# Performance work log

Hardware: AMD Instinct MI355X
Metric: run time of the kernel (lower is better)

The kernel has to match this reference:

```python
import jax, jax.numpy as jnp
import numpy as np

N_EMBD = 1024
N_HEAD = 16

def setup_inputs() -> dict:
    key = jax.random.key(0)
    ks = jax.random.split(key, 5)
    C = N_EMBD
    x = jax.random.normal(ks[0], (4, 2048, C), dtype=jnp.float32)
    s = 1.0 / np.sqrt(C)
    W_attn = jax.random.normal(ks[1], (C, 3 * C), dtype=jnp.float32) * s
    b_attn = jnp.zeros((3 * C,), dtype=jnp.float32)
    W_proj = jax.random.normal(ks[2], (C, C), dtype=jnp.float32) * s
    b_proj = jnp.zeros((C,), dtype=jnp.float32)
    return {"x": x, "W_attn": W_attn, "b_attn": b_attn, "W_proj": W_proj, "b_proj": b_proj}

def reference(x, W_attn, b_attn, W_proj, b_proj):
    B, S, C = x.shape
    Nh = N_HEAD
    Ne = C // Nh
    qkv = x @ W_attn + b_attn                      # [B,S,3C]
    q, k, v = jnp.split(qkv, 3, axis=-1)
    def heads(t):
        return t.reshape(B, S, Nh, Ne).transpose(0, 2, 1, 3)  # [B,Nh,S,Ne]
    q, k, v = heads(q), heads(k), heads(v)
    scale = 1.0 / np.sqrt(Ne)
    att = scale * jnp.einsum('bhqe,bhke->bhqk', q, k)          # [B,Nh,S,S]
    mask = jnp.tril(jnp.ones((S, S), dtype=bool))
    att = jnp.where(mask, att, -jnp.inf)
    att = jax.nn.softmax(att, axis=-1)
    y = jnp.einsum('bhqk,bhke->bhqe', att, v)                  # [B,Nh,S,Ne]
    y = y.transpose(0, 2, 1, 3).reshape(B, S, C)
    return y @ W_proj + b_proj
```

## Files before the change

### kernel.cpp

```cpp
#include <hip/hip_runtime.h>
#include <cstdint>
#include <cstddef>

typedef _Float16 h16;
typedef _Float16 h16x4 __attribute__((ext_vector_type(4)));
typedef _Float16 h16x8 __attribute__((ext_vector_type(8)));
typedef __fp16 fp16x2 __attribute__((ext_vector_type(2)));
typedef float f32x4 __attribute__((ext_vector_type(4)));

#define LOG2E 1.44269504088896f
#define QSCALE (0.125f * LOG2E)
#define THR 11.0f

static __device__ __forceinline__ f32x4 mfma_f16(h16x8 a, h16x8 b, f32x4 c) {
  return __builtin_amdgcn_mfma_f32_16x16x32_f16(a, b, c, 0, 0, 0);
}

static __device__ __forceinline__ void gload_lds16(const void* g, void* s) {
  __builtin_amdgcn_global_load_lds(
      (__attribute__((address_space(1))) void*)(uintptr_t)g,
      (__attribute__((address_space(3))) void*)s, 16, 0, 0);
}

__global__ __launch_bounds__(256) void k_cvt(const float* __restrict__ in,
                                             h16* __restrict__ out, int n) {
  int i = (blockIdx.x * 256 + threadIdx.x) * 8;
  if (i >= n) return;
  float4 a = *(const float4*)(in + i);
  float4 b = *(const float4*)(in + i + 4);
  h16x8 o;
  o[0] = (h16)a.x; o[1] = (h16)a.y; o[2] = (h16)a.z; o[3] = (h16)a.w;
  o[4] = (h16)b.x; o[5] = (h16)b.y; o[6] = (h16)b.z; o[7] = (h16)b.w;
  *(h16x8*)(out + i) = o;
}

__global__ __launch_bounds__(256) void k_tr_cvt(const float* __restrict__ in,
                                                h16* __restrict__ out, int R, int C) {
  __shared__ float tile[32][33];
  int c0 = blockIdx.x * 32, r0 = blockIdx.y * 32;
  int tx = threadIdx.x & 31, ty = threadIdx.x >> 5;
#pragma unroll
  for (int i = 0; i < 4; i++) {
    int r = ty + i * 8;
    tile[r][tx] = in[(size_t)(r0 + r) * C + c0 + tx];
  }
  __syncthreads();
#pragma unroll
  for (int i = 0; i < 4; i++) {
    int c = ty + i * 8;
    out[(size_t)(c0 + c) * R + r0 + tx] = (h16)tile[tx][c];
  }
}

#define SLOT_H16 24576
#define NT_K 16

static __device__ __forceinline__ void gemm_main256(
    const h16* __restrict__ A, const h16* __restrict__ BT,
    int m0, int n0, h16* sAB, f32x4 acc[4][4]) {
  const int tid = threadIdx.x;
  const int lane = tid & 63, w = tid >> 6;
  const int lm = lane & 15, lh = lane >> 4;
  const int wr = w >> 1, wc = w & 1;
  const int wbase = w * 512;
  const int srow = tid >> 3;
  const int scol = (((tid & 7) ^ (srow & 7)) << 3);
  const h16* gA = A + (size_t)(m0 + srow) * 1024 + scol;
  const h16* gB = BT + (size_t)(n0 + srow) * 1024 + scol;

  auto stage = [&](int t, int sl) {
    const int k = t * 64;
    h16* d = sAB + sl * SLOT_H16 + wbase;
    gload_lds16(gA + (size_t)0 * 65536 + k, d + 0 * 4096);
    gload_lds16(gA + (size_t)1 * 65536 + k, d + 1 * 4096);
    gload_lds16(gA + (size_t)2 * 65536 + k, d + 2 * 4096);
    gload_lds16(gA + (size_t)3 * 65536 + k, d + 3 * 4096);
    gload_lds16(gB + (size_t)0 * 65536 + k, d + 16384 + 0 * 4096);
    gload_lds16(gB + (size_t)1 * 65536 + k, d + 16384 + 1 * 4096);
  };

  stage(0, 0);
  stage(1, 1);
  asm volatile("s_waitcnt vmcnt(6)" ::: "memory");
  __builtin_amdgcn_s_barrier();

  int sl = 0, ss = 2;
  for (int t = 0; t < NT_K; ++t) {
    if (t < NT_K - 2) stage(t + 2, ss);
    const h16* sa = sAB + sl * SLOT_H16;
    const h16* sb = sa + 16384;
    h16x8 af[4][2], bf[4][2];
#pragma unroll
    for (int mi = 0; mi < 4; mi++) {
      const int row = wr * 64 + mi * 16 + lm;
#pragma unroll
      for (int kk = 0; kk < 2; kk++)
        af[mi][kk] = *(const h16x8*)(sa + row * 64 + ((kk * 32 + lh * 8) ^ ((lm & 7) << 3)));
    }
#pragma unroll
    for (int ni = 0; ni < 4; ni++) {
      const int row = wc * 64 + ni * 16 + lm;
#pragma unroll
      for (int kk = 0; kk < 2; kk++)
        bf[ni][kk] = *(const h16x8*)(sb + row * 64 + ((kk * 32 + lh * 8) ^ ((lm & 7) << 3)));
    }
    __builtin_amdgcn_s_setprio(1);
#pragma unroll
    for (int mi = 0; mi < 4; mi++)
#pragma unroll
      for (int ni = 0; ni < 4; ni++)
        acc[mi][ni] = mfma_f16(af[mi][1], bf[ni][1],
                               mfma_f16(af[mi][0], bf[ni][0], acc[mi][ni]));
    __builtin_amdgcn_s_setprio(0);
    if (t < NT_K - 2) asm volatile("s_waitcnt vmcnt(6)" ::: "memory");
    else              asm volatile("s_waitcnt vmcnt(0)" ::: "memory");
    __builtin_amdgcn_s_barrier();
    sl = (sl == 2) ? 0 : sl + 1;
    ss = (ss == 2) ? 0 : ss + 1;
  }
}

__global__ __launch_bounds__(512, 2) void k_gemm_qkv(const h16* __restrict__ xb,
                                                     const h16* __restrict__ WTa,
                                                     const float* __restrict__ b_attn,
                                                     h16* __restrict__ qb,
                                                     h16* __restrict__ kbuf,
                                                     h16* __restrict__ vT) {
  __shared__ __align__(16) h16 sAB[3 * SLOT_H16];
  const int bid = blockIdx.x;
  const int flat = (bid & 7) * 96 + (bid >> 3);
  const int mt = flat / 24, nt = flat % 24;
  const int m0 = mt * 256, n0 = nt * 128;
  f32x4 acc[4][4];
#pragma unroll
  for (int i = 0; i < 4; i++)
#pragma unroll
    for (int j = 0; j < 4; j++) acc[i][j] = (f32x4){0.f, 0.f, 0.f, 0.f};
  gemm_main256(xb, WTa, m0, n0, sAB, acc);

  const int tid = threadIdx.x, lane = tid & 63, w = tid >> 6;
  const int lm = lane & 15, lh = lane >> 4;
  const int wr = w >> 1, wc = w & 1;
#pragma unroll
  for (int ni = 0; ni < 4; ni++) {
    const int n = n0 + wc * 64 + ni * 16 + lm;
    const float bias = b_attn[n];
    const int which = n >> 10, cc = n & 1023, hh = cc >> 6, e = cc & 63;
#pragma unroll
    for (int mi = 0; mi < 4; mi++) {
#pragma unroll
      for (int r = 0; r < 4; r++) {
        const int m = m0 + wr * 64 + mi * 16 + lh * 4 + r;
        const int b = m >> 11, s = m & 2047;
        const h16 o = (h16)(acc[mi][ni][r] + bias);
        const size_t bh = (size_t)(b * 16 + hh);
        if (which == 0)      qb[(bh * 2048 + s) * 64 + e] = o;
        else if (which == 1) kbuf[(bh * 2048 + s) * 64 + e] = o;
        else                 vT[(bh * 64 + e) * 2048 + s] = o;
      }
    }
  }
}

__global__ __launch_bounds__(512, 2) void k_gemm_proj(const h16* __restrict__ yb,
                                                      const h16* __restrict__ WTp,
                                                      const float* __restrict__ b_proj,
                                                      float* __restrict__ out) {
  __shared__ __align__(16) h16 sAB[3 * SLOT_H16];
  const int bid = blockIdx.x;
  const int flat = (bid & 7) * 32 + (bid >> 3);
  const int mt = flat / 8, nt = flat % 8;
  const int m0 = mt * 256, n0 = nt * 128;
  f32x4 acc[4][4];
#pragma unroll
  for (int i = 0; i < 4; i++)
#pragma unroll
    for (int j = 0; j < 4; j++) acc[i][j] = (f32x4){0.f, 0.f, 0.f, 0.f};
  gemm_main256(yb, WTp, m0, n0, sAB, acc);

  const int tid = threadIdx.x, lane = tid & 63, w = tid >> 6;
  const int lm = lane & 15, lh = lane >> 4;
  const int wr = w >> 1, wc = w & 1;
#pragma unroll
  for (int ni = 0; ni < 4; ni++) {
    const int n = n0 + wc * 64 + ni * 16 + lm;
    const float bias = b_proj[n];
#pragma unroll
    for (int mi = 0; mi < 4; mi++) {
#pragma unroll
      for (int r = 0; r < 4; r++) {
        const int m = m0 + wr * 64 + mi * 16 + lh * 4 + r;
        out[(size_t)m * 1024 + n] = acc[mi][ni][r] + bias;
      }
    }
  }
}

__global__ __launch_bounds__(256, 3) void k_attn(const h16* __restrict__ qb,
                                                 const h16* __restrict__ kbuf,
                                                 const h16* __restrict__ vT,
                                                 h16* __restrict__ yb) {
  __shared__ __align__(16) h16 sKt[2][64 * 64];
  __shared__ __align__(16) h16 sVt[2][64 * 64];
  __shared__ __align__(16) h16 sP[4][2][16 * 64];

  const int bid = blockIdx.x;
  const int bh = bid & 63;
  const int qt = 15 - (bid >> 6);
  const int b = bh >> 4, h = bh & 15;
  const int tid = threadIdx.x, lam = tid & 63, w = tid >> 6;
  const int lm = lam & 15, lh = lam >> 4;
  const int q0 = qt * 128 + w * 32;
  const h16* Q = qb + (size_t)bh * 2048 * 64;
  const h16* Kp = kbuf + (size_t)bh * 2048 * 64;
  const h16* Vp = vT + (size_t)bh * 64 * 2048;

  const int srow = lam >> 3;
  const int xo8 = (((lam & 7) ^ (srow & 7)) << 3);

  h16x8 qf[2][2];
#pragma unroll
  for (int rt = 0; rt < 2; rt++)
#pragma unroll
    for (int dc = 0; dc < 2; dc++) {
      h16x8 qv = *(const h16x8*)(Q + (size_t)(q0 + rt * 16 + lm) * 64 + dc * 32 + lh * 8);
      h16x8 o;
#pragma unroll
      for (int i = 0; i < 8; i++) o[i] = (h16)((float)qv[i] * QSCALE);
      qf[rt][dc] = o;
    }

  f32x4 yacc[2][4];
  float m2[2], lw[2];
#pragma unroll
  for (int rt = 0; rt < 2; rt++) {
    m2[rt] = -1e30f;
    lw[rt] = 0.f;
#pragma unroll
    for (int i = 0; i < 4; i++) yacc[rt][i] = (f32x4){0.f, 0.f, 0.f, 0.f};
  }

  const int nsteps = qt * 2 + 2;

#pragma unroll
  for (int i = 0; i < 2; i++) {
    const int seg = 2 * w + i;
    const int r = seg * 8 + srow;
    gload_lds16(Kp + (size_t)r * 64 + xo8, &sKt[0][seg * 512]);
    gload_lds16(Vp + (size_t)r * 2048 + xo8, &sVt[0][seg * 512]);
  }
  asm volatile("s_waitcnt vmcnt(0)" ::: "memory");
  __syncthreads();

  for (int tt = 0; tt < nsteps; ++tt) {
    const int kb0 = tt * 64, cur = tt & 1;
    if (tt + 1 < nsteps) {
      const int kn = kb0 + 64;
#pragma unroll
      for (int i = 0; i < 2; i++) {
        const int seg = 2 * w + i;
        const int r = seg * 8 + srow;
        gload_lds16(Kp + (size_t)(kn + r) * 64 + xo8, &sKt[cur ^ 1][seg * 512]);
        gload_lds16(Vp + (size_t)r * 2048 + kn + xo8, &sVt[cur ^ 1][seg * 512]);
      }
    }
    if (kb0 <= q0 + 31) {
      const bool domask = (kb0 + 63 > q0);
      h16x8 kf[4][2];
#pragma unroll
      for (int ct = 0; ct < 4; ct++)
#pragma unroll
        for (int dc = 0; dc < 2; dc++)
          kf[ct][dc] = *(const h16x8*)(
              &sKt[cur][(ct * 16 + lm) * 64 + ((dc * 32 + lh * 8) ^ ((lm & 7) << 3))]);
      h16x8 vf[4][2];
#pragma unroll
      for (int dt = 0; dt < 4; dt++)
#pragma unroll
        for (int kc = 0; kc < 2; kc++)
          vf[dt][kc] = *(const h16x8*)(
              &sVt[cur][(dt * 16 + lm) * 64 + ((kc * 32 + lh * 8) ^ ((lm & 7) << 3))]);

#pragma unroll
      for (int rt = 0; rt < 2; rt++) {
        const int qrow = q0 + rt * 16 + lm;
        f32x4 sv[4];
        __builtin_amdgcn_s_setprio(1);
#pragma unroll
        for (int ct = 0; ct < 4; ct++) {
          f32x4 s = mfma_f16(kf[ct][0], qf[rt][0], (f32x4){0.f, 0.f, 0.f, 0.f});
          sv[ct] = mfma_f16(kf[ct][1], qf[rt][1], s);
        }
        __builtin_amdgcn_s_setprio(0);
        if (domask) {
#pragma unroll
          for (int ct = 0; ct < 4; ct++)
#pragma unroll
            for (int r = 0; r < 4; r++)
              if (kb0 + ct * 16 + lh * 4 + r > qrow) sv[ct][r] = -1e30f;
        }
        float rm = fmaxf(fmaxf(fmaxf(sv[0][0], sv[0][1]), fmaxf(sv[0][2], sv[0][3])),
                         fmaxf(fmaxf(sv[1][0], sv[1][1]), fmaxf(sv[1][2], sv[1][3])));
        rm = fmaxf(rm, fmaxf(fmaxf(fmaxf(sv[2][0], sv[2][1]), fmaxf(sv[2][2], sv[2][3])),
                             fmaxf(fmaxf(sv[3][0], sv[3][1]), fmaxf(sv[3][2], sv[3][3]))));
        rm = fmaxf(rm, __shfl_xor(rm, 16));
        rm = fmaxf(rm, __shfl_xor(rm, 32));
        if (!__all(rm <= m2[rt] + THR)) {
          const float nm = fmaxf(m2[rt], rm);
          const float alpha = __builtin_amdgcn_exp2f(m2[rt] - nm);
          m2[rt] = nm;
          lw[rt] *= alpha;
#pragma unroll
          for (int dt = 0; dt < 4; dt++) yacc[rt][dt] *= alpha;
        }
        const float m = m2[rt];
        float psum = 0.f;
#pragma unroll
        for (int ct = 0; ct < 4; ct++) {
          const float p0 = __builtin_amdgcn_exp2f(sv[ct][0] - m);
          const float p1 = __builtin_amdgcn_exp2f(sv[ct][1] - m);
          const float p2 = __builtin_amdgcn_exp2f(sv[ct][2] - m);
          const float p3 = __builtin_amdgcn_exp2f(sv[ct][3] - m);
          psum += (p0 + p1) + (p2 + p3);
          const fp16x2 u0 = __builtin_amdgcn_cvt_pkrtz(p0, p1);
          const fp16x2 u1 = __builtin_amdgcn_cvt_pkrtz(p2, p3);
          const int base = ct * 16 + lh * 4;
          *(fp16x2*)(&sP[w][rt][lm * 64 + ((base + 0) ^ ((lm & 7) << 3))]) = u0;
          *(fp16x2*)(&sP[w][rt][lm * 64 + ((base + 2) ^ ((lm & 7) << 3))]) = u1;
        }
        lw[rt] += psum;
      }
#pragma unroll
      for (int rt = 0; rt < 2; rt++) {
        const h16x8 pf0 = *(const h16x8*)(
            &sP[w][rt][lm * 64 + ((lh * 8) ^ ((lm & 7) << 3))]);
        const h16x8 pf1 = *(const h16x8*)(
            &sP[w][rt][lm * 64 + ((32 + lh * 8) ^ ((lm & 7) << 3))]);
        __builtin_amdgcn_s_setprio(1);
#pragma unroll
        for (int dt = 0; dt < 4; dt++) {
          f32x4 y = mfma_f16(vf[dt][0], pf0, yacc[rt][dt]);
          yacc[rt][dt] = mfma_f16(vf[dt][1], pf1, y);
        }
        __builtin_amdgcn_s_setprio(0);
      }
    }
    asm volatile("s_waitcnt vmcnt(0)" ::: "memory");
    __syncthreads();
  }

#pragma unroll
  for (int rt = 0; rt < 2; rt++) {
    float s = lw[rt];
    s += __shfl_xor(s, 16);
    s += __shfl_xor(s, 32);
    const float inv = 1.0f / s;
    const int q = q0 + rt * 16 + lm;
    const size_t yrow = ((size_t)b * 2048 + q) * 1024 + h * 64;
#pragma unroll
    for (int dt = 0; dt < 4; dt++) {
      h16x4 o;
#pragma unroll
      for (int r = 0; r < 4; r++) o[r] = (h16)(yacc[rt][dt][r] * inv);
      *(h16x4*)(yb + yrow + dt * 16 + lh * 4) = o;
    }
  }
}

extern "C" void kernel_launch(void* const* d_in, const int* in_sizes, int n_in,
                              void* d_out, int out_size, void* d_ws, size_t ws_size,
                              hipStream_t stream) {
  const float* x      = (const float*)d_in[0];
  const float* W_attn = (const float*)d_in[1];
  const float* b_attn = (const float*)d_in[2];
  const float* W_proj = (const float*)d_in[3];
  const float* b_proj = (const float*)d_in[4];
  float* out = (float*)d_out;

  char* ws = (char*)d_ws;
  h16* xb   = (h16*)(ws);
  h16* WTa  = (h16*)(ws + 16777216);
  h16* WTp  = (h16*)(ws + 23068672);
  h16* qb   = (h16*)(ws + 25165824);
  h16* kbuf = (h16*)(ws + 41943040);
  h16* vT   = (h16*)(ws + 58720256);
  h16* yb   = xb;

  k_cvt<<<dim3(8192 * 1024 / 2048), 256, 0, stream>>>(x, xb, 8192 * 1024);
  k_tr_cvt<<<dim3(3072 / 32, 1024 / 32), 256, 0, stream>>>(W_attn, WTa, 1024, 3072);
  k_tr_cvt<<<dim3(1024 / 32, 1024 / 32), 256, 0, stream>>>(W_proj, WTp, 1024, 1024);
  k_gemm_qkv<<<dim3(768), 512, 0, stream>>>(xb, WTa, b_attn, qb, kbuf, vT);
  k_attn<<<dim3(64 * 16), 256, 0, stream>>>(qb, kbuf, vT, yb);
  k_gemm_proj<<<dim3(256), 512, 0, stream>>>(yb, WTp, b_proj, out);
}
```

Baseline: 290.9 us.

## Enlarge GEMM tiles to 256x256 with 4-stage K=32 pipeline and split compute phases

Both GEMMs now use 256x256 output tiles per 512-thread block (8 waves as 2x4, 128x64 per wave) instead of 256x128, halving the grid sizes. The K loop uses 32-wide slices with a four-slot LDS ring and three stages in flight, and splits each iteration into two MFMA phases separated by barriers to interleave LDS reads with compute. This aims for more reuse per loaded byte and better latency hiding, at the cost of occupancy of one block per CU and fewer blocks (128 for proj) than CUs on the device.

```diff
diff --git a/kernel.cpp b/kernel.cpp
--- a/kernel.cpp
+++ b/kernel.cpp
@@ -52,105 +52,123 @@
   }
 }
 
-#define SLOT_H16 24576
-#define NT_K 16
-
-static __device__ __forceinline__ void gemm_main256(
-    const h16* __restrict__ A, const h16* __restrict__ BT,
-    int m0, int n0, h16* sAB, f32x4 acc[4][4]) {
+#define SLOT_E 16384
+#define NTK 32
+
+static __device__ __forceinline__ void gemm8p(const h16* __restrict__ A,
+                                              const h16* __restrict__ BT,
+                                              int m0, int n0, h16* sAB,
+                                              f32x4 acc[8][4]) {
   const int tid = threadIdx.x;
   const int lane = tid & 63, w = tid >> 6;
   const int lm = lane & 15, lh = lane >> 4;
-  const int wr = w >> 1, wc = w & 1;
-  const int wbase = w * 512;
-  const int srow = tid >> 3;
-  const int scol = (((tid & 7) ^ (srow & 7)) << 3);
-  const h16* gA = A + (size_t)(m0 + srow) * 1024 + scol;
-  const h16* gB = BT + (size_t)(n0 + srow) * 1024 + scol;
-
-  auto stage = [&](int t, int sl) {
-    const int k = t * 64;
-    h16* d = sAB + sl * SLOT_H16 + wbase;
-    gload_lds16(gA + (size_t)0 * 65536 + k, d + 0 * 4096);
-    gload_lds16(gA + (size_t)1 * 65536 + k, d + 1 * 4096);
-    gload_lds16(gA + (size_t)2 * 65536 + k, d + 2 * 4096);
-    gload_lds16(gA + (size_t)3 * 65536 + k, d + 3 * 4096);
-    gload_lds16(gB + (size_t)0 * 65536 + k, d + 16384 + 0 * 4096);
-    gload_lds16(gB + (size_t)1 * 65536 + k, d + 16384 + 1 * 4096);
+  const int wr = w >> 2, wc = w & 3;
+  const int rdx = (lm >> 1) & 3;
+
+  const h16* pA[2];
+  const h16* pB[2];
+  int dst[2];
+#pragma unroll
+  for (int r = 0; r < 2; r++) {
+    const int idx = tid + r * 512;
+    const int srow = idx >> 2;
+    const int gsrc = (idx & 3) ^ ((srow >> 1) & 3);
+    pA[r] = A + (size_t)(m0 + srow) * 1024 + gsrc * 8;
+    pB[r] = BT + (size_t)(n0 + srow) * 1024 + gsrc * 8;
+    dst[r] = w * 512 + r * 4096;
+  }
+
+  auto stage = [&](int kt) {
+    h16* slot = sAB + (kt & 3) * SLOT_E;
+    const int k0 = kt * 32;
+#pragma unroll
+    for (int r = 0; r < 2; r++) {
+      gload_lds16(pA[r] + k0, slot + dst[r]);
+      gload_lds16(pB[r] + k0, slot + 8192 + dst[r]);
+    }
   };
 
-  stage(0, 0);
-  stage(1, 1);
-  asm volatile("s_waitcnt vmcnt(6)" ::: "memory");
+  stage(0); stage(1); stage(2);
+  asm volatile("s_waitcnt vmcnt(8)" ::: "memory");
   __builtin_amdgcn_s_barrier();
 
-  int sl = 0, ss = 2;
-  for (int t = 0; t < NT_K; ++t) {
-    if (t < NT_K - 2) stage(t + 2, ss);
-    const h16* sa = sAB + sl * SLOT_H16;
-    const h16* sb = sa + 16384;
-    h16x8 af[4][2], bf[4][2];
-#pragma unroll
-    for (int mi = 0; mi < 4; mi++) {
-      const int row = wr * 64 + mi * 16 + lm;
-#pragma unroll
-      for (int kk = 0; kk < 2; kk++)
-        af[mi][kk] = *(const h16x8*)(sa + row * 64 + ((kk * 32 + lh * 8) ^ ((lm & 7) << 3)));
-    }
-#pragma unroll
-    for (int ni = 0; ni < 4; ni++) {
-      const int row = wc * 64 + ni * 16 + lm;
-#pragma unroll
-      for (int kk = 0; kk < 2; kk++)
-        bf[ni][kk] = *(const h16x8*)(sb + row * 64 + ((kk * 32 + lh * 8) ^ ((lm & 7) << 3)));
-    }
+  for (int kt = 0; kt < NTK; ++kt) {
+    if (kt + 3 < NTK) stage(kt + 3);
+    const h16* sa = sAB + (kt & 3) * SLOT_E;
+    const h16* sb = sa + 8192;
+
+    h16x8 af[4], bf[4];
+#pragma unroll
+    for (int mi = 0; mi < 4; mi++)
+      af[mi] = *(const h16x8*)(sa + (wr * 128 + mi * 16 + lm) * 32 + ((lh ^ rdx) << 3));
+#pragma unroll
+    for (int ni = 0; ni < 4; ni++)
+      bf[ni] = *(const h16x8*)(sb + (wc * 64 + ni * 16 + lm) * 32 + ((lh ^ rdx) << 3));
+    __builtin_amdgcn_sched_barrier(0);
+    __builtin_amdgcn_s_barrier();
+    asm volatile("s_waitcnt lgkmcnt(0)" ::: "memory");
     __builtin_amdgcn_s_setprio(1);
 #pragma unroll
     for (int mi = 0; mi < 4; mi++)
 #pragma unroll
       for (int ni = 0; ni < 4; ni++)
-        acc[mi][ni] = mfma_f16(af[mi][1], bf[ni][1],
-                               mfma_f16(af[mi][0], bf[ni][0], acc[mi][ni]));
+        acc[mi][ni] = mfma_f16(af[mi], bf[ni], acc[mi][ni]);
     __builtin_amdgcn_s_setprio(0);
-    if (t < NT_K - 2) asm volatile("s_waitcnt vmcnt(6)" ::: "memory");
-    else              asm volatile("s_waitcnt vmcnt(0)" ::: "memory");
     __builtin_amdgcn_s_barrier();
-    sl = (sl == 2) ? 0 : sl + 1;
-    ss = (ss == 2) ? 0 : ss + 1;
-  }
-}
-
-__global__ __launch_bounds__(512, 2) void k_gemm_qkv(const h16* __restrict__ xb,
+
+    h16x8 ag[4];
+#pragma unroll
+    for (int mi = 0; mi < 4; mi++)
+      ag[mi] = *(const h16x8*)(sa + (wr * 128 + (mi + 4) * 16 + lm) * 32 + ((lh ^ rdx) << 3));
+    __builtin_amdgcn_sched_barrier(0);
+    __builtin_amdgcn_s_barrier();
+    asm volatile("s_waitcnt lgkmcnt(0)" ::: "memory");
+    __builtin_amdgcn_s_setprio(1);
+#pragma unroll
+    for (int mi = 0; mi < 4; mi++)
+#pragma unroll
+      for (int ni = 0; ni < 4; ni++)
+        acc[mi + 4][ni] = mfma_f16(ag[mi], bf[ni], acc[mi + 4][ni]);
+    __builtin_amdgcn_s_setprio(0);
+
+    if (kt < NTK - 3)      asm volatile("s_waitcnt vmcnt(8)" ::: "memory");
+    else if (kt == NTK - 3) asm volatile("s_waitcnt vmcnt(4)" ::: "memory");
+    else if (kt == NTK - 2) asm volatile("s_waitcnt vmcnt(0)" ::: "memory");
+    __builtin_amdgcn_s_barrier();
+  }
+}
+
+__global__ __launch_bounds__(512, 1) void k_gemm_qkv(const h16* __restrict__ xb,
                                                      const h16* __restrict__ WTa,
                                                      const float* __restrict__ b_attn,
                                                      h16* __restrict__ qb,
                                                      h16* __restrict__ kbuf,
                                                      h16* __restrict__ vT) {
-  __shared__ __align__(16) h16 sAB[3 * SLOT_H16];
+  __shared__ __align__(16) h16 sAB[4 * SLOT_E];
   const int bid = blockIdx.x;
-  const int flat = (bid & 7) * 96 + (bid >> 3);
-  const int mt = flat / 24, nt = flat % 24;
-  const int m0 = mt * 256, n0 = nt * 128;
-  f32x4 acc[4][4];
-#pragma unroll
-  for (int i = 0; i < 4; i++)
+  const int flat = (bid & 7) * 48 + (bid >> 3);
+  const int mt = flat / 12, nt = flat % 12;
+  const int m0 = mt * 256, n0 = nt * 256;
+  f32x4 acc[8][4];
+#pragma unroll
+  for (int i = 0; i < 8; i++)
 #pragma unroll
     for (int j = 0; j < 4; j++) acc[i][j] = (f32x4){0.f, 0.f, 0.f, 0.f};
-  gemm_main256(xb, WTa, m0, n0, sAB, acc);
+  gemm8p(xb, WTa, m0, n0, sAB, acc);
 
   const int tid = threadIdx.x, lane = tid & 63, w = tid >> 6;
   const int lm = lane & 15, lh = lane >> 4;
-  const int wr = w >> 1, wc = w & 1;
+  const int wr = w >> 2, wc = w & 3;
 #pragma unroll
   for (int ni = 0; ni < 4; ni++) {
     const int n = n0 + wc * 64 + ni * 16 + lm;
     const float bias = b_attn[n];
     const int which = n >> 10, cc = n & 1023, hh = cc >> 6, e = cc & 63;
 #pragma unroll
-    for (int mi = 0; mi < 4; mi++) {
+    for (int mi = 0; mi < 8; mi++) {
 #pragma unroll
       for (int r = 0; r < 4; r++) {
-        const int m = m0 + wr * 64 + mi * 16 + lh * 4 + r;
+        const int m = m0 + wr * 128 + mi * 16 + lh * 4 + r;
         const int b = m >> 11, s = m & 2047;
         const h16 o = (h16)(acc[mi][ni][r] + bias);
         const size_t bh = (size_t)(b * 16 + hh);
@@ -162,34 +180,34 @@
   }
 }
 
-__global__ __launch_bounds__(512, 2) void k_gemm_proj(const h16* __restrict__ yb,
+__global__ __launch_bounds__(512, 1) void k_gemm_proj(const h16* __restrict__ yb,
                                                       const h16* __restrict__ WTp,
                                                       const float* __restrict__ b_proj,
                                                       float* __restrict__ out) {
-  __shared__ __align__(16) h16 sAB[3 * SLOT_H16];
+  __shared__ __align__(16) h16 sAB[4 * SLOT_E];
   const int bid = blockIdx.x;
-  const int flat = (bid & 7) * 32 + (bid >> 3);
-  const int mt = flat / 8, nt = flat % 8;
-  const int m0 = mt * 256, n0 = nt * 128;
-  f32x4 acc[4][4];
-#pragma unroll
-  for (int i = 0; i < 4; i++)
+  const int flat = (bid & 7) * 16 + (bid >> 3);
+  const int mt = flat / 4, nt = flat % 4;
+  const int m0 = mt * 256, n0 = nt * 256;
+  f32x4 acc[8][4];
+#pragma unroll
+  for (int i = 0; i < 8; i++)
 #pragma unroll
     for (int j = 0; j < 4; j++) acc[i][j] = (f32x4){0.f, 0.f, 0.f, 0.f};
-  gemm_main256(yb, WTp, m0, n0, sAB, acc);
+  gemm8p(yb, WTp, m0, n0, sAB, acc);
 
   const int tid = threadIdx.x, lane = tid & 63, w = tid >> 6;
   const int lm = lane & 15, lh = lane >> 4;
-  const int wr = w >> 1, wc = w & 1;
+  const int wr = w >> 2, wc = w & 3;
 #pragma unroll
   for (int ni = 0; ni < 4; ni++) {
     const int n = n0 + wc * 64 + ni * 16 + lm;
     const float bias = b_proj[n];
 #pragma unroll
-    for (int mi = 0; mi < 4; mi++) {
+    for (int mi = 0; mi < 8; mi++) {
 #pragma unroll
       for (int r = 0; r < 4; r++) {
-        const int m = m0 + wr * 64 + mi * 16 + lh * 4 + r;
+        const int m = m0 + wr * 128 + mi * 16 + lh * 4 + r;
         out[(size_t)m * 1024 + n] = acc[mi][ni][r] + bias;
       }
     }
@@ -389,7 +407,7 @@
   k_cvt<<<dim3(8192 * 1024 / 2048), 256, 0, stream>>>(x, xb, 8192 * 1024);
   k_tr_cvt<<<dim3(3072 / 32, 1024 / 32), 256, 0, stream>>>(W_attn, WTa, 1024, 3072);
   k_tr_cvt<<<dim3(1024 / 32, 1024 / 32), 256, 0, stream>>>(W_proj, WTp, 1024, 1024);
-  k_gemm_qkv<<<dim3(768), 512, 0, stream>>>(xb, WTa, b_attn, qb, kbuf, vT);
+  k_gemm_qkv<<<dim3(384), 512, 0, stream>>>(xb, WTa, b_attn, qb, kbuf, vT);
   k_attn<<<dim3(64 * 16), 256, 0, stream>>>(qb, kbuf, vT, yb);
-  k_gemm_proj<<<dim3(256), 512, 0, stream>>>(yb, WTp, b_proj, out);
-}
+  k_gemm_proj<<<dim3(128), 512, 0, stream>>>(yb, WTp, b_proj, out);
+}
```

Measured after the change: 314.1 us. 8.0% more time.
